# Optimization experiments

Measured on AMD Instinct MI355X. Metric: run time of the kernel, lower is better.

Reference implementation:

```python
import math
import jax, jax.numpy as jnp
import numpy as np

B, S, D = 4, 2048, 1024
N_HEAD = 16


def setup_inputs() -> dict:
    key = jax.random.key(0)
    k1, k2 = jax.random.split(key)
    x = jax.random.normal(k1, (B, S, D), dtype=jnp.float32)
    # xavier-uniform style scale for the fused QKV kernel
    limit = math.sqrt(6.0 / (D + 3 * D))
    W_qkv = jax.random.uniform(k2, (D, 3 * D), dtype=jnp.float32, minval=-limit, maxval=limit)
    b_qkv = jnp.zeros((3 * D,), dtype=jnp.float32)
    return {"x": x, "W_qkv": W_qkv, "b_qkv": b_qkv}


def reference(x, W_qkv, b_qkv):
    batch_size, seq_len, d_model = x.shape
    head_dim = d_model // N_HEAD
    # fused QKV projection: [B, S, 3D]
    qkv = jnp.einsum('bsd,de->bse', x, W_qkv) + b_qkv
    qkv = qkv.reshape(batch_size, seq_len, N_HEAD, 3 * head_dim)
    qkv = qkv.transpose(0, 2, 1, 3)  # [B, H, S, 3*hd]
    q, k, v = jnp.split(qkv, 3, axis=-1)
    # scaled dot-product attention with causal mask
    attn_logits = jnp.einsum('bhqd,bhkd->bhqk', q, k) / math.sqrt(head_dim)
    causal = jnp.tril(jnp.ones((seq_len, seq_len), dtype=jnp.float32))[None, None]
    attn_logits = jnp.where(causal == 0, -jnp.inf, attn_logits)
    attn = jax.nn.softmax(attn_logits, axis=-1)
    out = jnp.einsum('bhqk,bhkd->bhqd', attn, v)  # [B, H, S, hd]
    out = out.transpose(0, 2, 1, 3).reshape(batch_size, seq_len, -1)
    return out
```

## Files before the change

kernel.cpp:

```cpp
#include <hip/hip_runtime.h>
#include <hip/hip_bf16.h>
#include <cstdint>

typedef __bf16 bf16x8 __attribute__((ext_vector_type(8)));
typedef float f32x4 __attribute__((ext_vector_type(4)));

__device__ inline unsigned short f2bf(float f) {
    union { float f; unsigned int u; } v; v.f = f;
    unsigned int u = v.u;
    unsigned int r = (u + 0x7FFFu + ((u >> 16) & 1u)) >> 16;
    return (unsigned short)r;
}

__device__ inline f32x4 mfma16(bf16x8 a, bf16x8 b, f32x4 c) {
    return __builtin_amdgcn_mfma_f32_16x16x32_bf16(a, b, c, 0, 0, 0);
}

__device__ inline bf16x8 ldfrag(const unsigned short* p) {
    uint4 v = *(const uint4*)p;
    return __builtin_bit_cast(bf16x8, v);
}

__device__ inline void cp16(const unsigned short* g, unsigned short* l) {
    __builtin_amdgcn_global_load_lds(
        (const __attribute__((address_space(1))) unsigned int*)g,
        (__attribute__((address_space(3))) unsigned int*)l,
        16, 0, 0);
}

__device__ inline unsigned int pkbf(float a, float b) {
    return __builtin_amdgcn_perm(__builtin_bit_cast(unsigned int, b),
                                 __builtin_bit_cast(unsigned int, a),
                                 0x07060302u);
}

__global__ void k_convert_x(const float* __restrict__ in,
                            unsigned short* __restrict__ out, int n4) {
    int i = blockIdx.x * blockDim.x + threadIdx.x;
    if (i < n4) {
        float4 f = ((const float4*)in)[i];
        ushort4 o;
        o.x = f2bf(f.x); o.y = f2bf(f.y); o.z = f2bf(f.z); o.w = f2bf(f.w);
        ((ushort4*)out)[i] = o;
    }
}

__global__ void k_transpose_w(const float* __restrict__ W,
                              unsigned short* __restrict__ Wt) {
    __shared__ float tile[32][33];
    int nt = blockIdx.x, kt = blockIdx.y;
    int tx = threadIdx.x & 31, ty = threadIdx.x >> 5;
#pragma unroll
    for (int yy = 0; yy < 4; ++yy) {
        int y = ty + yy * 8;
        tile[y][tx] = W[(size_t)(kt * 32 + y) * 3072 + nt * 32 + tx];
    }
    __syncthreads();
#pragma unroll
    for (int yy = 0; yy < 4; ++yy) {
        int nrow = ty + yy * 8;
        Wt[(size_t)(nt * 32 + nrow) * 1024 + kt * 32 + tx] = f2bf(tile[tx][nrow]);
    }
}

__global__ __launch_bounds__(256) void k_qkv_gemm(
    const unsigned short* __restrict__ A,
    const unsigned short* __restrict__ Bt,
    const float* __restrict__ bias,
    unsigned short* __restrict__ C) {
    __shared__ unsigned short As[128 * 32];
    __shared__ unsigned short Bs[128 * 32];
    const int tid = threadIdx.x;
    const int lane = tid & 63;
    const int w = tid >> 6;
    const int wm = w >> 1, wn = w & 1;
    const int l15 = lane & 15;
    const int quad = lane >> 4;
    const int m0 = blockIdx.y * 128;
    const int n0 = blockIdx.x * 128;

    f32x4 acc[4][4] = {};

    for (int k0 = 0; k0 < 1024; k0 += 32) {
#pragma unroll
        for (int i = 0; i < 2; ++i) {
            int c = tid + i * 256;
            int row = c >> 2, seg = c & 3;
            cp16(A + (size_t)(m0 + row) * 1024 + k0 + seg * 8, &As[c * 8]);
            cp16(Bt + (size_t)(n0 + row) * 1024 + k0 + seg * 8, &Bs[c * 8]);
        }
        __syncthreads();
        const int col8 = quad * 8;
        bf16x8 af[4], bfr[4];
#pragma unroll
        for (int i = 0; i < 4; ++i)
            af[i] = ldfrag(As + (wm * 64 + i * 16 + l15) * 32 + col8);
#pragma unroll
        for (int j = 0; j < 4; ++j)
            bfr[j] = ldfrag(Bs + (wn * 64 + j * 16 + l15) * 32 + col8);
#pragma unroll
        for (int i = 0; i < 4; ++i)
#pragma unroll
            for (int j = 0; j < 4; ++j)
                acc[i][j] = mfma16(af[i], bfr[j], acc[i][j]);
        __syncthreads();
    }
#pragma unroll
    for (int i = 0; i < 4; ++i) {
#pragma unroll
        for (int j = 0; j < 4; ++j) {
            int col = n0 + wn * 64 + j * 16 + l15;
            float bv = bias[col];
#pragma unroll
            for (int r = 0; r < 4; ++r) {
                int row = m0 + wm * 64 + i * 16 + quad * 4 + r;
                C[(size_t)row * 3072 + col] = f2bf(acc[i][j][r] + bv);
            }
        }
    }
}

__global__ __launch_bounds__(256) void k_transpose_v(
    const unsigned short* __restrict__ qkv,
    unsigned short* __restrict__ VtG) {
    __shared__ unsigned short t[64][65];
    const int st = blockIdx.x;
    const int h = blockIdx.y;
    const int b = blockIdx.z;
    const int tid = threadIdx.x;
    const int voff = h * 192 + 128;
    const size_t base = (size_t)b * 2048 * 3072;
#pragma unroll
    for (int i = 0; i < 2; ++i) {
        int c = tid + i * 256;
        int row = c >> 3, seg = c & 7;
        uint4 v = *(const uint4*)(qkv + base + (size_t)(st * 64 + row) * 3072 + voff + seg * 8);
        unsigned short u8[8];
        *(uint4*)u8 = v;
#pragma unroll
        for (int u = 0; u < 8; ++u) t[row][seg * 8 + u] = u8[u];
    }
    __syncthreads();
    const size_t obase = ((size_t)(b * 16 + h) * 64) * 2048 + st * 64;
#pragma unroll
    for (int i = 0; i < 2; ++i) {
        int c = tid + i * 256;
        int drow = c >> 3, seg = c & 7;
        unsigned short u8[8];
#pragma unroll
        for (int u = 0; u < 8; ++u) u8[u] = t[seg * 8 + u][drow];
        *(uint4*)(VtG + obase + (size_t)drow * 2048 + seg * 8) = *(uint4*)u8;
    }
}

__global__ __launch_bounds__(256) void k_attn(
    const unsigned short* __restrict__ qkv,
    const unsigned short* __restrict__ VtG,
    float* __restrict__ out) {
    const int p = blockIdx.x;
    const int hb = p & 63;
    const int h = hb & 15;
    const int b = hb >> 4;
    const int qt_hi = 31 - (p >> 6);
    const int qt_lo = p >> 6;
    const int tid = threadIdx.x;
    const int lane = tid & 63;
    const int w = tid >> 6;
    const int l15 = lane & 15;
    const int quad = lane >> 4;

    __shared__ unsigned short KsF[2 * 64 * 64];
    __shared__ unsigned short VsF[2 * 64 * 64];
    __shared__ unsigned short PsF[4 * 16 * 64];

    const size_t base = (size_t)b * 2048 * 3072;
    const int qoff = h * 192, koff = h * 192 + 64;
    const size_t vtbase = (size_t)(b * 16 + h) * 64 * 2048;

    const int srow0 = tid >> 3, sseg = tid & 7;
    const int swz8 = (sseg ^ (srow0 & 7)) * 8;
    unsigned short* kd0 = &KsF[srow0 * 64 + swz8];
    unsigned short* kd1 = &KsF[(srow0 + 32) * 64 + swz8];
    unsigned short* vd0 = &VsF[srow0 * 64 + swz8];
    unsigned short* vd1 = &VsF[(srow0 + 32) * 64 + swz8];

    const int xr = l15 & 7;
    const int rb0 = (quad ^ xr) * 8;
    const int rb1 = ((quad + 4) ^ xr) * 8;

    const float sc = 0.125f * 1.44269504088896340736f;
    const int pwbase = w * 1024 + l15 * 64;
    unsigned short* prd = &PsF[pwbase];

    auto run_item = [&](int qt) {
        const int qbw = qt * 64 + w * 16;
        const unsigned short* qp =
            qkv + base + (size_t)(qbw + l15) * 3072 + qoff + quad * 8;
        const bf16x8 bq0 = ldfrag(qp);
        const bf16x8 bq1 = ldfrag(qp + 32);

        const unsigned short* kp0 = qkv + base + koff + sseg * 8 + (size_t)srow0 * 3072;
        const unsigned short* kp1 = kp0 + (size_t)32 * 3072;
        const unsigned short* vp0 = VtG + vtbase + (size_t)srow0 * 2048 + sseg * 8;
        const unsigned short* vp1 = vp0 + (size_t)32 * 2048;

        f32x4 o[4] = {};
        float ptot = 0.f;

        uint4 kr0 = *(const uint4*)kp0;
        uint4 kr1 = *(const uint4*)kp1;
        uint4 vr0 = *(const uint4*)vp0;
        uint4 vr1 = *(const uint4*)vp1;

        __syncthreads();

        for (int kt = 0; kt <= qt; ++kt) {
            const int bo = (kt & 1) * 4096;
            *(uint4*)(kd0 + bo) = kr0;
            *(uint4*)(kd1 + bo) = kr1;
            *(uint4*)(vd0 + bo) = vr0;
            *(uint4*)(vd1 + bo) = vr1;
            if (kt < qt) {
                kp0 += 64 * 3072; kp1 += 64 * 3072;
                vp0 += 64;        vp1 += 64;
                kr0 = *(const uint4*)kp0;
                kr1 = *(const uint4*)kp1;
                vr0 = *(const uint4*)vp0;
                vr1 = *(const uint4*)vp1;
            }
            __syncthreads();

            f32x4 s[4];
#pragma unroll
            for (int j = 0; j < 4; ++j) {
                const unsigned short* kr = &KsF[bo + (j * 16 + l15) * 64];
                f32x4 z = {0.f, 0.f, 0.f, 0.f};
                z = mfma16(ldfrag(kr + rb0), bq0, z);
                z = mfma16(ldfrag(kr + rb1), bq1, z);
                s[j] = z;
            }

            if (kt == qt) {
                const int qrel = w * 16 + l15;
#pragma unroll
                for (int j = 0; j < 4; ++j) {
                    const int sb = j * 16 + quad * 4;
#pragma unroll
                    for (int r = 0; r < 4; ++r)
                        if (sb + r > qrel) s[j][r] = -3.0e38f;
                }
            }

#pragma unroll
            for (int j = 0; j < 4; ++j) {
                float pv[4];
#pragma unroll
                for (int r = 0; r < 4; ++r) {
                    pv[r] = __builtin_amdgcn_exp2f(
                        __builtin_fmaf(s[j][r], sc, -16.0f));
                    ptot += pv[r];
                }
                unsigned int lo = pkbf(pv[0], pv[1]);
                unsigned int hi = pkbf(pv[2], pv[3]);
                const int sblk = (j * 2 + (quad >> 1)) ^ xr;
                uint2 pk; pk.x = lo; pk.y = hi;
                *(uint2*)&PsF[pwbase + sblk * 8 + (quad & 1) * 4] = pk;
            }

            bf16x8 bp0 = ldfrag(prd + rb0);
            bf16x8 bp1 = ldfrag(prd + rb1);
#pragma unroll
            for (int jd = 0; jd < 4; ++jd) {
                const unsigned short* vr = &VsF[bo + (jd * 16 + l15) * 64];
                o[jd] = mfma16(ldfrag(vr + rb0), bp0, o[jd]);
                o[jd] = mfma16(ldfrag(vr + rb1), bp1, o[jd]);
            }
        }

        float l = ptot;
        l += __shfl_xor(l, 16, 64);
        l += __shfl_xor(l, 32, 64);
        const float inv = __builtin_amdgcn_rcpf(l);
        float* op = out + ((size_t)b * 2048 + qbw + l15) * 1024 + h * 64 + quad * 4;
#pragma unroll
        for (int jd = 0; jd < 4; ++jd) {
            float4 v;
            v.x = o[jd][0] * inv; v.y = o[jd][1] * inv;
            v.z = o[jd][2] * inv; v.w = o[jd][3] * inv;
            *(float4*)(op + jd * 16) = v;
        }
    };

    run_item(qt_hi);
    run_item(qt_lo);
}

extern "C" void kernel_launch(void* const* d_in, const int* in_sizes, int n_in,
                              void* d_out, int out_size, void* d_ws, size_t ws_size,
                              hipStream_t stream) {
    const float* x = (const float*)d_in[0];
    const float* W = (const float*)d_in[1];
    const float* bq = (const float*)d_in[2];
    float* out = (float*)d_out;

    unsigned short* xbf = (unsigned short*)d_ws;
    unsigned short* wtbf = xbf + (size_t)8192 * 1024;
    unsigned short* qkvbf = wtbf + (size_t)3072 * 1024;
    unsigned short* VtG = xbf;

    k_convert_x<<<8192, 256, 0, stream>>>(x, xbf, 8192 * 1024 / 4);
    k_transpose_w<<<dim3(96, 32), 256, 0, stream>>>(W, wtbf);
    k_qkv_gemm<<<dim3(24, 64), 256, 0, stream>>>(xbf, wtbf, bq, qkvbf);
    k_transpose_v<<<dim3(32, 16, 4), 256, 0, stream>>>(qkvbf, VtG);
    k_attn<<<1024, 256, 0, stream>>>(qkvbf, VtG, out);
}
```

Measured before the change: 232.0 us.

## Fuse prep kernels, write Q/K/Vt directly from GEMM epilogue, single-buffer attention LDS

Merges the x conversion and W transpose into one launch, and has the QKV GEMM epilogue scatter into separate Q and K buffers plus a pre-transposed V buffer. This removes the separate V-transpose kernel and an intermediate round trip through global memory. The attention kernel now reads compact Q/K rows, single-buffers its K/V shared memory with an extra barrier per tile, and requests higher occupancy through launch bounds. The trade-offs are strided 2-byte stores in the GEMM epilogue, more workspace, and a serialized LDS store/compute step that relies on occupancy to hide latency.

```diff
diff --git a/kernel.cpp b/kernel.cpp
--- a/kernel.cpp
+++ b/kernel.cpp
@@ -34,32 +34,32 @@
                                  0x07060302u);
 }
 
-__global__ void k_convert_x(const float* __restrict__ in,
-                            unsigned short* __restrict__ out, int n4) {
-    int i = blockIdx.x * blockDim.x + threadIdx.x;
-    if (i < n4) {
-        float4 f = ((const float4*)in)[i];
+__global__ __launch_bounds__(256) void k_prep(
+    const float* __restrict__ x, const float* __restrict__ W,
+    unsigned short* __restrict__ xbf, unsigned short* __restrict__ wtbf) {
+    int bid = blockIdx.x;
+    if (bid < 8192) {
+        int i = bid * 256 + threadIdx.x;
+        float4 f = ((const float4*)x)[i];
         ushort4 o;
         o.x = f2bf(f.x); o.y = f2bf(f.y); o.z = f2bf(f.z); o.w = f2bf(f.w);
-        ((ushort4*)out)[i] = o;
-    }
-}
-
-__global__ void k_transpose_w(const float* __restrict__ W,
-                              unsigned short* __restrict__ Wt) {
-    __shared__ float tile[32][33];
-    int nt = blockIdx.x, kt = blockIdx.y;
-    int tx = threadIdx.x & 31, ty = threadIdx.x >> 5;
-#pragma unroll
-    for (int yy = 0; yy < 4; ++yy) {
-        int y = ty + yy * 8;
-        tile[y][tx] = W[(size_t)(kt * 32 + y) * 3072 + nt * 32 + tx];
-    }
-    __syncthreads();
-#pragma unroll
-    for (int yy = 0; yy < 4; ++yy) {
-        int nrow = ty + yy * 8;
-        Wt[(size_t)(nt * 32 + nrow) * 1024 + kt * 32 + tx] = f2bf(tile[tx][nrow]);
+        ((ushort4*)xbf)[i] = o;
+    } else {
+        bid -= 8192;
+        __shared__ float tile[32][33];
+        int nt = bid % 96, kt = bid / 96;
+        int tx = threadIdx.x & 31, ty = threadIdx.x >> 5;
+#pragma unroll
+        for (int yy = 0; yy < 4; ++yy) {
+            int y = ty + yy * 8;
+            tile[y][tx] = W[(size_t)(kt * 32 + y) * 3072 + nt * 32 + tx];
+        }
+        __syncthreads();
+#pragma unroll
+        for (int yy = 0; yy < 4; ++yy) {
+            int nrow = ty + yy * 8;
+            wtbf[(size_t)(nt * 32 + nrow) * 1024 + kt * 32 + tx] = f2bf(tile[tx][nrow]);
+        }
     }
 }
 
@@ -67,7 +67,9 @@
     const unsigned short* __restrict__ A,
     const unsigned short* __restrict__ Bt,
     const float* __restrict__ bias,
-    unsigned short* __restrict__ C) {
+    unsigned short* __restrict__ Qb,
+    unsigned short* __restrict__ Kb,
+    unsigned short* __restrict__ VtG) {
     __shared__ unsigned short As[128 * 32];
     __shared__ unsigned short Bs[128 * 32];
     const int tid = threadIdx.x;
@@ -105,56 +107,45 @@
                 acc[i][j] = mfma16(af[i], bfr[j], acc[i][j]);
         __syncthreads();
     }
-#pragma unroll
-    for (int i = 0; i < 4; ++i) {
-#pragma unroll
-        for (int j = 0; j < 4; ++j) {
-            int col = n0 + wn * 64 + j * 16 + l15;
-            float bv = bias[col];
-#pragma unroll
-            for (int r = 0; r < 4; ++r) {
-                int row = m0 + wm * 64 + i * 16 + quad * 4 + r;
-                C[(size_t)row * 3072 + col] = f2bf(acc[i][j][r] + bv);
+
+    const int m_b = m0 >> 11;
+    const int s0 = (m0 & 2047) + wm * 64 + quad * 4;
+#pragma unroll
+    for (int j = 0; j < 4; ++j) {
+        const int cj = n0 + wn * 64 + j * 16;
+        const int hh = cj / 192;
+        const int c192 = cj - hh * 192;
+        const float bv = bias[cj + l15];
+        if (c192 < 128) {
+            unsigned short* dst = (c192 < 64 ? Qb : Kb);
+            const int coff = hh * 64 + (c192 & 63) + l15;
+#pragma unroll
+            for (int i = 0; i < 4; ++i) {
+                const int mrow = m0 + wm * 64 + i * 16 + quad * 4;
+#pragma unroll
+                for (int r = 0; r < 4; ++r)
+                    dst[(size_t)(mrow + r) * 1024 + coff] = f2bf(acc[i][j][r] + bv);
+            }
+        } else {
+            const int d = c192 - 128 + l15;
+            unsigned short* vrow =
+                VtG + ((size_t)(m_b * 16 + hh) * 64 + d) * 2048;
+#pragma unroll
+            for (int i = 0; i < 4; ++i) {
+                ushort4 pk;
+                pk.x = f2bf(acc[i][j][0] + bv);
+                pk.y = f2bf(acc[i][j][1] + bv);
+                pk.z = f2bf(acc[i][j][2] + bv);
+                pk.w = f2bf(acc[i][j][3] + bv);
+                *(ushort4*)(vrow + s0 + i * 16) = pk;
             }
         }
     }
 }
 
-__global__ __launch_bounds__(256) void k_transpose_v(
-    const unsigned short* __restrict__ qkv,
-    unsigned short* __restrict__ VtG) {
-    __shared__ unsigned short t[64][65];
-    const int st = blockIdx.x;
-    const int h = blockIdx.y;
-    const int b = blockIdx.z;
-    const int tid = threadIdx.x;
-    const int voff = h * 192 + 128;
-    const size_t base = (size_t)b * 2048 * 3072;
-#pragma unroll
-    for (int i = 0; i < 2; ++i) {
-        int c = tid + i * 256;
-        int row = c >> 3, seg = c & 7;
-        uint4 v = *(const uint4*)(qkv + base + (size_t)(st * 64 + row) * 3072 + voff + seg * 8);
-        unsigned short u8[8];
-        *(uint4*)u8 = v;
-#pragma unroll
-        for (int u = 0; u < 8; ++u) t[row][seg * 8 + u] = u8[u];
-    }
-    __syncthreads();
-    const size_t obase = ((size_t)(b * 16 + h) * 64) * 2048 + st * 64;
-#pragma unroll
-    for (int i = 0; i < 2; ++i) {
-        int c = tid + i * 256;
-        int drow = c >> 3, seg = c & 7;
-        unsigned short u8[8];
-#pragma unroll
-        for (int u = 0; u < 8; ++u) u8[u] = t[seg * 8 + u][drow];
-        *(uint4*)(VtG + obase + (size_t)drow * 2048 + seg * 8) = *(uint4*)u8;
-    }
-}
-
-__global__ __launch_bounds__(256) void k_attn(
-    const unsigned short* __restrict__ qkv,
+__global__ __launch_bounds__(256, 6) void k_attn(
+    const unsigned short* __restrict__ Qb,
+    const unsigned short* __restrict__ Kb,
     const unsigned short* __restrict__ VtG,
     float* __restrict__ out) {
     const int p = blockIdx.x;
@@ -169,13 +160,13 @@
     const int l15 = lane & 15;
     const int quad = lane >> 4;
 
-    __shared__ unsigned short KsF[2 * 64 * 64];
-    __shared__ unsigned short VsF[2 * 64 * 64];
+    __shared__ unsigned short KsF[64 * 64];
+    __shared__ unsigned short VsF[64 * 64];
     __shared__ unsigned short PsF[4 * 16 * 64];
 
-    const size_t base = (size_t)b * 2048 * 3072;
-    const int qoff = h * 192, koff = h * 192 + 64;
+    const size_t rbase = (size_t)b * 2048;
     const size_t vtbase = (size_t)(b * 16 + h) * 64 * 2048;
+    const int hoff = h * 64;
 
     const int srow0 = tid >> 3, sseg = tid & 7;
     const int swz8 = (sseg ^ (srow0 & 7)) * 8;
@@ -195,12 +186,12 @@
     auto run_item = [&](int qt) {
         const int qbw = qt * 64 + w * 16;
         const unsigned short* qp =
-            qkv + base + (size_t)(qbw + l15) * 3072 + qoff + quad * 8;
+            Qb + (rbase + qbw + l15) * 1024 + hoff + quad * 8;
         const bf16x8 bq0 = ldfrag(qp);
         const bf16x8 bq1 = ldfrag(qp + 32);
 
-        const unsigned short* kp0 = qkv + base + koff + sseg * 8 + (size_t)srow0 * 3072;
-        const unsigned short* kp1 = kp0 + (size_t)32 * 3072;
+        const unsigned short* kp0 = Kb + (rbase + srow0) * 1024 + hoff + sseg * 8;
+        const unsigned short* kp1 = kp0 + (size_t)32 * 1024;
         const unsigned short* vp0 = VtG + vtbase + (size_t)srow0 * 2048 + sseg * 8;
         const unsigned short* vp1 = vp0 + (size_t)32 * 2048;
 
@@ -212,16 +203,14 @@
         uint4 vr0 = *(const uint4*)vp0;
         uint4 vr1 = *(const uint4*)vp1;
 
-        __syncthreads();
-
         for (int kt = 0; kt <= qt; ++kt) {
-            const int bo = (kt & 1) * 4096;
-            *(uint4*)(kd0 + bo) = kr0;
-            *(uint4*)(kd1 + bo) = kr1;
-            *(uint4*)(vd0 + bo) = vr0;
-            *(uint4*)(vd1 + bo) = vr1;
+            __syncthreads();
+            *(uint4*)kd0 = kr0;
+            *(uint4*)kd1 = kr1;
+            *(uint4*)vd0 = vr0;
+            *(uint4*)vd1 = vr1;
             if (kt < qt) {
-                kp0 += 64 * 3072; kp1 += 64 * 3072;
+                kp0 += 64 * 1024; kp1 += 64 * 1024;
                 vp0 += 64;        vp1 += 64;
                 kr0 = *(const uint4*)kp0;
                 kr1 = *(const uint4*)kp1;
@@ -233,7 +222,7 @@
             f32x4 s[4];
 #pragma unroll
             for (int j = 0; j < 4; ++j) {
-                const unsigned short* kr = &KsF[bo + (j * 16 + l15) * 64];
+                const unsigned short* kr = &KsF[(j * 16 + l15) * 64];
                 f32x4 z = {0.f, 0.f, 0.f, 0.f};
                 z = mfma16(ldfrag(kr + rb0), bq0, z);
                 z = mfma16(ldfrag(kr + rb1), bq1, z);
@@ -271,7 +260,7 @@
             bf16x8 bp1 = ldfrag(prd + rb1);
 #pragma unroll
             for (int jd = 0; jd < 4; ++jd) {
-                const unsigned short* vr = &VsF[bo + (jd * 16 + l15) * 64];
+                const unsigned short* vr = &VsF[(jd * 16 + l15) * 64];
                 o[jd] = mfma16(ldfrag(vr + rb0), bp0, o[jd]);
                 o[jd] = mfma16(ldfrag(vr + rb1), bp1, o[jd]);
             }
@@ -281,7 +270,7 @@
         l += __shfl_xor(l, 16, 64);
         l += __shfl_xor(l, 32, 64);
         const float inv = __builtin_amdgcn_rcpf(l);
-        float* op = out + ((size_t)b * 2048 + qbw + l15) * 1024 + h * 64 + quad * 4;
+        float* op = out + (rbase + qbw + l15) * 1024 + hoff + quad * 4;
 #pragma unroll
         for (int jd = 0; jd < 4; ++jd) {
             float4 v;
@@ -305,12 +294,11 @@
 
     unsigned short* xbf = (unsigned short*)d_ws;
     unsigned short* wtbf = xbf + (size_t)8192 * 1024;
-    unsigned short* qkvbf = wtbf + (size_t)3072 * 1024;
-    unsigned short* VtG = xbf;
-
-    k_convert_x<<<8192, 256, 0, stream>>>(x, xbf, 8192 * 1024 / 4);
-    k_transpose_w<<<dim3(96, 32), 256, 0, stream>>>(W, wtbf);
-    k_qkv_gemm<<<dim3(24, 64), 256, 0, stream>>>(xbf, wtbf, bq, qkvbf);
-    k_transpose_v<<<dim3(32, 16, 4), 256, 0, stream>>>(qkvbf, VtG);
-    k_attn<<<1024, 256, 0, stream>>>(qkvbf, VtG, out);
-}
+    unsigned short* Qb = wtbf + (size_t)3072 * 1024;
+    unsigned short* Kb = Qb + (size_t)8192 * 1024;
+    unsigned short* VtG = Kb + (size_t)8192 * 1024;
+
+    k_prep<<<8192 + 3072, 256, 0, stream>>>(x, W, xbf, wtbf);
+    k_qkv_gemm<<<dim3(24, 64), 256, 0, stream>>>(xbf, wtbf, bq, Qb, Kb, VtG);
+    k_attn<<<1024, 256, 0, stream>>>(Qb, Kb, VtG, out);
+}
```

After: 248.8 us. 7.2% more time.
